# Kernel tuning notes

Hardware: AMD Instinct MI355X
Metric: run time of the kernel (lower is better)

The kernel has to match this reference:

```python
import jax, jax.numpy as jnp
import numpy as np

EPS = 1e-12  # torch F.normalize eps


def setup_inputs() -> dict:
    key = jax.random.key(0)
    k1, k2, k3, k4, k5 = jax.random.split(key, 5)
    N, C, H, W = 32, 512, 32, 32
    E = 1024   # expansion * dim
    G = 8      # group
    D = E // G # 128, per-group channel dim
    K = 64     # num_clusters
    x = jax.random.normal(k1, (N, C, H, W), dtype=jnp.float32)
    W1 = jax.random.normal(k2, (E, C), dtype=jnp.float32) / np.sqrt(C)
    W2 = jax.random.normal(k3, (G, E), dtype=jnp.float32) / np.sqrt(E)
    Wc = jax.random.normal(k4, (K, D), dtype=jnp.float32) / np.sqrt(D)
    centroids = jax.random.uniform(k5, (K, D), dtype=jnp.float32)
    return {"x": x, "W1": W1, "W2": W2, "Wc": Wc, "centroids": centroids}


def reference(x, W1, W2, Wc, centroids):
    # x: [N, C, H, W]; W1: [E, C]; W2: [G, E]; Wc: [K, D]; centroids: [K, D]
    N, C, H, W = x.shape
    E = W1.shape[0]
    G = W2.shape[0]
    K, D = Wc.shape
    P = H * W
    # descriptor-wise L2 normalization over channel dim
    norm = jnp.linalg.norm(x, axis=1, keepdims=True)
    x = x / jnp.maximum(norm, EPS)
    # linear1 on channels: [N, E, P]
    xe = jnp.einsum('ncp,ec->nep', x.reshape(N, C, P), W1)
    # grouped features: [N, G, D, P]
    xg = xe.reshape(N, G, D, P)
    # attention gate: sigmoid(linear2)  -> [N, G, P]
    att = jax.nn.sigmoid(jnp.einsum('nep,ge->ngp', xe, W2))
    # 1x1 conv = per-pixel matmul with cluster weights -> [N, G, K, P]
    soft_assign = jax.nn.softmax(jnp.einsum('ngdp,kd->ngkp', xg, Wc), axis=2)
    # combined per-(cluster,pixel) weight
    w = soft_assign * att[:, :, None, :]  # [N, G, K, P]
    # NetVLAD residual aggregation, algebraically decomposed to avoid the
    # giant [N,G,K,D,P] intermediate:
    #   vlad[n,k,d] = sum_{g,p} w * xg  -  centroids[k,d] * sum_{g,p} w
    agg = jnp.einsum('ngkp,ngdp->nkd', w, xg)  # [N, K, D]
    wsum = w.sum(axis=(1, 3))                  # [N, K]
    vlad = agg - wsum[:, :, None] * centroids[None]  # [N, K, D]
    return vlad.reshape(N, K * D)
```

## Files before the change

kernel.cpp:

```cpp
#include <hip/hip_runtime.h>


#define N_  32
#define C_  512
#define P_  1024
#define E_  1024
#define G_  8
#define D_  128
#define K_  64

typedef __attribute__((ext_vector_type(8))) short bf16x8;
typedef __attribute__((ext_vector_type(4))) float f32x4;

__device__ __forceinline__ unsigned short f2b(float f) {
    union { float f; unsigned u; } v; v.f = f;
    unsigned r = (v.u + 0x7FFFu + ((v.u >> 16) & 1u)) >> 16;
    return (unsigned short)r;
}
__device__ __forceinline__ float b2f(unsigned short h) {
    union { unsigned u; float f; } v; v.u = ((unsigned)h) << 16;
    return v.f;
}

__device__ __forceinline__ void gl_lds16(const void* g, void* l) {
    __builtin_amdgcn_global_load_lds(
        (const __attribute__((address_space(1))) void*)g,
        (__attribute__((address_space(3))) void*)l, 16, 0, 0);
}

#define SB  __builtin_amdgcn_sched_barrier(0)
#define BAR __builtin_amdgcn_s_barrier()

__global__ __launch_bounds__(256) void k0_prep(const float* __restrict__ W1,
                                               const float* __restrict__ Wc,
                                               unsigned short* __restrict__ W1b,
                                               unsigned short* __restrict__ Vb) {
    int bid = blockIdx.x;
    int t = threadIdx.x;
    int i0 = bid * 512 + t;
    W1b[i0]       = f2b(W1[i0]);
    W1b[i0 + 256] = f2b(W1[i0 + 256]);
    int ch = bid & 1, k = (bid >> 1) & 63, g = bid >> 7;
    int c = ch * 256 + t;
    float acc = 0.f;
    #pragma unroll 8
    for (int d = 0; d < 128; ++d)
        acc += Wc[k * 128 + d] * W1[(g * 128 + d) * C_ + c];
    Vb[(g * 64 + k) * C_ + c] = f2b(acc);
}

__global__ __launch_bounds__(256) void k1_norm_transpose(const float* __restrict__ x,
                                                         unsigned short* __restrict__ xhat_t) {
    __shared__ short xc[128 * 256];
    __shared__ float red[256];
    __shared__ float rn[64];
    int n = blockIdx.y;
    int p0 = blockIdx.x * 64;
    int t = threadIdx.x;
    int ps = t & 63, cs = t >> 6;

    float ss = 0.f;
    for (int i = 0; i < 128; ++i) {
        float v = x[((size_t)(n * C_ + cs * 128 + i)) * P_ + p0 + ps];
        ss += v * v;
        xc[i * 256 + t] = (short)f2b(v);
    }
    red[t] = ss;
    __syncthreads();
    if (t < 64) {
        float s = red[t] + red[64 + t] + red[128 + t] + red[192 + t];
        rn[t] = 1.0f / fmaxf(sqrtf(s), 1e-12f);
    }
    __syncthreads();

    float r = rn[ps];
    size_t base = ((size_t)(n * P_ + p0 + ps)) * C_ + cs * 128;
    #pragma unroll
    for (int jj = 0; jj < 16; ++jj) {
        bf16x8 o;
        #pragma unroll
        for (int j = 0; j < 8; ++j)
            o[j] = (short)f2b(b2f((unsigned short)xc[(jj * 8 + j) * 256 + t]) * r);
        *(bf16x8*)&xhat_t[base + jj * 8] = o;
    }
}

__global__ __launch_bounds__(256) void k2_gemm_xe(const unsigned short* __restrict__ W1b,
                                                  const unsigned short* __restrict__ xhat_t,
                                                  unsigned short* __restrict__ xe) {
    __shared__ __align__(16) short As[128 * 64];
    __shared__ __align__(16) short Bs[128 * 64];
    int n = blockIdx.y;
    int e0 = (blockIdx.x >> 3) * 128;
    int p0 = (blockIdx.x & 7) * 128;
    int t = threadIdx.x;
    int w = t >> 6, l = t & 63, q = l >> 4, l15 = l & 15;
    int wr = w >> 1, wc = w & 1;

    f32x4 acc[4][4];
    #pragma unroll
    for (int mi = 0; mi < 4; ++mi)
        #pragma unroll
        for (int ni = 0; ni < 4; ++ni)
            acc[mi][ni] = (f32x4){0.f, 0.f, 0.f, 0.f};

    for (int ks = 0; ks < 8; ++ks) {
        int k0 = ks * 64;
        #pragma unroll
        for (int i = 0; i < 4; ++i) {
            int ch = i * 256 + t;
            int row = ch >> 3, c8 = ch & 7;
            gl_lds16(&W1b[(e0 + row) * C_ + k0 + ((c8 ^ (row & 7)) * 8)], &As[ch * 8]);
        }
        #pragma unroll
        for (int i = 0; i < 4; ++i) {
            int ch = i * 256 + t;
            int row = ch >> 3, c8 = ch & 7;
            gl_lds16(&xhat_t[((size_t)(n * P_ + p0 + row)) * C_ + k0 + ((c8 ^ (row & 7)) * 8)], &Bs[ch * 8]);
        }
        __syncthreads();

        #pragma unroll
        for (int kk = 0; kk < 2; ++kk) {
            bf16x8 af[4], bf[4];
            #pragma unroll
            for (int mi = 0; mi < 4; ++mi)
                af[mi] = *(const bf16x8*)&As[(wr * 64 + mi * 16 + l15) * 64 + (((kk * 4 + q) ^ (l15 & 7)) * 8)];
            #pragma unroll
            for (int ni = 0; ni < 4; ++ni)
                bf[ni] = *(const bf16x8*)&Bs[(wc * 64 + ni * 16 + l15) * 64 + (((kk * 4 + q) ^ (l15 & 7)) * 8)];
            #pragma unroll
            for (int mi = 0; mi < 4; ++mi)
                #pragma unroll
                for (int ni = 0; ni < 4; ++ni)
                    acc[mi][ni] = __builtin_amdgcn_mfma_f32_16x16x32_bf16(af[mi], bf[ni], acc[mi][ni], 0, 0, 0);
        }
        __syncthreads();
    }

    #pragma unroll
    for (int mi = 0; mi < 4; ++mi) {
        #pragma unroll
        for (int ni = 0; ni < 4; ++ni) {
            #pragma unroll
            for (int r = 0; r < 4; ++r) {
                int e = e0 + wr * 64 + mi * 16 + q * 4 + r;
                int p = p0 + wc * 64 + ni * 16 + l15;
                xe[((size_t)(n * E_ + e)) * P_ + p] = f2b(acc[mi][ni][r]);
            }
        }
    }
}

__global__ __launch_bounds__(256) void k3a_att_part(const unsigned short* __restrict__ xe,
                                                    const float* __restrict__ W2,
                                                    float* __restrict__ att_part) {
    int n = blockIdx.y;
    int ec = blockIdx.x;
    int t = threadIdx.x;
    int e0 = ec * 64;
    f32x4 acc[8];
    #pragma unroll
    for (int g = 0; g < 8; ++g) acc[g] = (f32x4){0.f, 0.f, 0.f, 0.f};
    #pragma unroll 4
    for (int i = 0; i < 64; ++i) {
        int e = e0 + i;
        ushort4 v4 = *(const ushort4*)&xe[((size_t)(n * E_ + e)) * P_ + t * 4];
        f32x4 vf = {b2f(v4.x), b2f(v4.y), b2f(v4.z), b2f(v4.w)};
        #pragma unroll
        for (int g = 0; g < 8; ++g)
            acc[g] += vf * W2[g * E_ + e];
    }
    #pragma unroll
    for (int g = 0; g < 8; ++g)
        *(f32x4*)&att_part[(((size_t)(n * 16 + ec)) * 8 + g) * P_ + t * 4] = acc[g];
}

__global__ __launch_bounds__(256) void k3b_att_reduce(const float* __restrict__ att_part,
                                                      float* __restrict__ att_s) {
    int idx = blockIdx.x * 256 + threadIdx.x;
    int p = idx & 1023;
    int g = (idx >> 10) & 7;
    int n = idx >> 13;
    float s = 0.f;
    #pragma unroll
    for (int ec = 0; ec < 16; ++ec)
        s += att_part[(((size_t)(n * 16 + ec)) * 8 + g) * P_ + p];
    att_s[idx] = 1.0f / (1.0f + __expf(-s));
}

__device__ __forceinline__ void stage_s(short* sb, const unsigned short* __restrict__ Vb,
                                        const unsigned short* __restrict__ xhat_t,
                                        int g, int n, int p0c, int k0, int t) {
    {
        int row = t >> 3, c8 = t & 7;
        gl_lds16(&Vb[(g * 64 + row) * C_ + k0 + ((c8 ^ (row & 7)) * 8)], &sb[t * 8]);
    }
    #pragma unroll
    for (int i = 0; i < 2; ++i) {
        int ch = i * 512 + t;
        int row = ch >> 3, c8 = ch & 7;
        gl_lds16(&xhat_t[((size_t)(n * P_ + p0c + row)) * C_ + k0 + ((c8 ^ (row & 7)) * 8)],
                 &sb[4096 + ch * 8]);
    }
}

__device__ __forceinline__ void stage_xg(short* xglds, const unsigned short* __restrict__ xe,
                                         int n, int g, int p0c, int t) {
    #pragma unroll
    for (int i = 0; i < 4; ++i) {
        int ch = i * 512 + t;
        int row = ch >> 4, c16 = ch & 15;
        gl_lds16(&xe[((size_t)(n * E_ + g * 128 + row)) * P_ + p0c + ((c16 ^ (row & 7)) * 8)],
                 &xglds[ch * 8]);
    }
}

__device__ __forceinline__ void mfma_s(f32x4 acc[4], const short* sb, int w, int q, int l15) {
    #pragma unroll
    for (int kk = 0; kk < 2; ++kk) {
        bf16x8 af[4], bfr;
        #pragma unroll
        for (int mi = 0; mi < 4; ++mi)
            af[mi] = *(const bf16x8*)&sb[(mi * 16 + l15) * 64 + (((kk * 4 + q) ^ (l15 & 7)) * 8)];
        bfr = *(const bf16x8*)&sb[4096 + (w * 16 + l15) * 64 + (((kk * 4 + q) ^ (l15 & 7)) * 8)];
        #pragma unroll
        for (int mi = 0; mi < 4; ++mi)
            acc[mi] = __builtin_amdgcn_mfma_f32_16x16x32_bf16(af[mi], bfr, acc[mi], 0, 0, 0);
    }
}

__global__ __launch_bounds__(512, 4) void k4_assign_agg(const unsigned short* __restrict__ Vb,
                                                        const unsigned short* __restrict__ xhat_t,
                                                        const unsigned short* __restrict__ xe,
                                                        const float* __restrict__ att_s,
                                                        float* __restrict__ agg_part,
                                                        float* __restrict__ wsum_part) {
    __shared__ __align__(16) char smem[81920];
    short* S0    = (short*)smem;
    short* S1    = (short*)(smem + 24576);
    short* xglds = (short*)(smem + 49152);
    short* wlds  = (short*)smem;
    float* wred  = (float*)smem;

    int b = blockIdx.y * 16 + blockIdx.x;
    int work = (b & 7) * 64 + (b >> 3);
    int n = work >> 4, g = work & 7, ph = (work >> 3) & 1;

    int t = threadIdx.x;
    int w = t >> 6, l = t & 63, q = l >> 4, l15 = l & 15;
    int kh = w >> 2, dq = w & 3;

    f32x4 acc_a[2][2];
    #pragma unroll
    for (int mi = 0; mi < 2; ++mi)
        #pragma unroll
        for (int ni = 0; ni < 2; ++ni)
            acc_a[mi][ni] = (f32x4){0.f, 0.f, 0.f, 0.f};
    float wsp[16];
    #pragma unroll
    for (int j = 0; j < 16; ++j) wsp[j] = 0.f;

#define WAITV(n_) asm volatile("s_waitcnt vmcnt(" #n_ ")" ::: "memory")
#define RND(CUR, NXT, KN) \
    stage_s(NXT, Vb, xhat_t, g, n, p0c, (KN) * 64, t); \
    WAITV(3); BAR; SB; \
    mfma_s(acc_s, CUR, w, q, l15); \
    BAR; SB;

    #pragma unroll 1
    for (int cc = 0; cc < 4; ++cc) {
        int p0c = ph * 512 + cc * 128;

        float av = att_s[(((size_t)(n * G_ + g)) * P_) + p0c + w * 16 + l15];

        f32x4 acc_s[4];
        #pragma unroll
        for (int mi = 0; mi < 4; ++mi)
            acc_s[mi] = (f32x4){0.f, 0.f, 0.f, 0.f};

        stage_s(S0, Vb, xhat_t, g, n, p0c, 0, t);
        RND(S0, S1, 1)
        RND(S1, S0, 2)
        RND(S0, S1, 3)
        RND(S1, S0, 4)
        RND(S0, S1, 5)
        RND(S1, S0, 6)
        stage_s(S1, Vb, xhat_t, g, n, p0c, 448, t);
        stage_xg(xglds, xe, n, g, p0c, t);
        WAITV(7); BAR; SB;
        mfma_s(acc_s, S0, w, q, l15);
        BAR; SB;
        WAITV(4); BAR; SB;
        mfma_s(acc_s, S1, w, q, l15);
        BAR; SB;

        {
            float m = -1e30f;
            #pragma unroll
            for (int mi = 0; mi < 4; ++mi)
                #pragma unroll
                for (int r = 0; r < 4; ++r)
                    m = fmaxf(m, acc_s[mi][r]);
            m = fmaxf(m, __shfl_xor(m, 16));
            m = fmaxf(m, __shfl_xor(m, 32));
            float s = 0.f;
            #pragma unroll
            for (int mi = 0; mi < 4; ++mi)
                #pragma unroll
                for (int r = 0; r < 4; ++r) {
                    float e = __expf(acc_s[mi][r] - m);
                    acc_s[mi][r] = e;
                    s += e;
                }
            s += __shfl_xor(s, 16);
            s += __shfl_xor(s, 32);

            float scale = av / s;

            #pragma unroll
            for (int mi = 0; mi < 4; ++mi)
                #pragma unroll
                for (int r = 0; r < 4; ++r) {
                    float wv = acc_s[mi][r] * scale;
                    wsp[mi * 4 + r] += wv;
                    wlds[(mi * 16 + q * 4 + r) * 136 + (w * 16 + l15)] = (short)f2b(wv);
                }
        }
        __syncthreads();

        #pragma unroll
        for (int pk = 0; pk < 4; ++pk) {
            bf16x8 a2[2], b2[2];
            #pragma unroll
            for (int mi = 0; mi < 2; ++mi)
                a2[mi] = *(const bf16x8*)&wlds[(kh * 32 + mi * 16 + l15) * 136 + pk * 32 + q * 8];
            #pragma unroll
            for (int ni = 0; ni < 2; ++ni)
                b2[ni] = *(const bf16x8*)&xglds[(dq * 32 + ni * 16 + l15) * 128
                                                + (((pk * 4 + q) ^ (l15 & 7)) * 8)];
            #pragma unroll
            for (int mi = 0; mi < 2; ++mi)
                #pragma unroll
                for (int ni = 0; ni < 2; ++ni)
                    acc_a[mi][ni] = __builtin_amdgcn_mfma_f32_16x16x32_bf16(a2[mi], b2[ni], acc_a[mi][ni], 0, 0, 0);
        }
        __syncthreads();
    }

    size_t base = (((size_t)(n * G_ + g)) * 2 + ph) * 64;
    #pragma unroll
    for (int mi = 0; mi < 2; ++mi)
        #pragma unroll
        for (int ni = 0; ni < 2; ++ni)
            #pragma unroll
            for (int r = 0; r < 4; ++r) {
                int k = kh * 32 + mi * 16 + q * 4 + r;
                int d = dq * 32 + ni * 16 + l15;
                agg_part[(base + k) * 128 + d] = acc_a[mi][ni][r];
            }

    #pragma unroll
    for (int j = 0; j < 16; ++j) {
        float v = wsp[j];
        v += __shfl_xor(v, 1);
        v += __shfl_xor(v, 2);
        v += __shfl_xor(v, 4);
        v += __shfl_xor(v, 8);
        if (l15 == 0) {
            int k = (j >> 2) * 16 + q * 4 + (j & 3);
            wred[w * 64 + k] = v;
        }
    }
    __syncthreads();
    if (t < 64) {
        float s = 0.f;
        #pragma unroll
        for (int wv = 0; wv < 8; ++wv)
            s += wred[wv * 64 + t];
        wsum_part[(((size_t)(n * G_ + g)) * 2 + ph) * 64 + t] = s;
    }
}

__global__ __launch_bounds__(256) void k5_final(const float* __restrict__ agg_part,
                                                const float* __restrict__ wsum_part,
                                                const float* __restrict__ centroids,
                                                float* __restrict__ out) {
    int idx = blockIdx.x * 256 + threadIdx.x;
    int d = idx & 127;
    int k = (idx >> 7) & 63;
    int n = idx >> 13;
    float ws = 0.f;
    #pragma unroll
    for (int g = 0; g < 8; ++g)
        #pragma unroll
        for (int ph = 0; ph < 2; ++ph)
            ws += wsum_part[(((size_t)(n * G_ + g)) * 2 + ph) * 64 + k];
    float agg = 0.f;
    #pragma unroll
    for (int g = 0; g < 8; ++g)
        #pragma unroll
        for (int ph = 0; ph < 2; ++ph)
            agg += agg_part[(((((size_t)(n * G_ + g)) * 2 + ph) * 64) + k) * 128 + d];
    out[idx] = agg - ws * centroids[k * 128 + d];
}

extern "C" void kernel_launch(void* const* d_in, const int* in_sizes, int n_in,
                              void* d_out, int out_size, void* d_ws, size_t ws_size,
                              hipStream_t stream) {
    const float* x         = (const float*)d_in[0];
    const float* W1        = (const float*)d_in[1];
    const float* W2        = (const float*)d_in[2];
    const float* Wc        = (const float*)d_in[3];
    const float* centroids = (const float*)d_in[4];
    float* out = (float*)d_out;

    char* ws = (char*)d_ws;
    unsigned short* W1b      = (unsigned short*)(ws + 0);
    unsigned short* Vb       = (unsigned short*)(ws + 1048576);
    unsigned short* xhat_t   = (unsigned short*)(ws + 1572864);
    unsigned short* xe       = (unsigned short*)(ws + 35127296);
    float*          att_s    = (float*)(ws + 102236160);
    float*          att_part = (float*)(ws + 103284736);
    float*          agg_part = (float*)(ws + 103284736);
    float*          wsum_part= (float*)(ws + 120061952);

    hipLaunchKernelGGL(k0_prep,        dim3(1024), dim3(256), 0, stream, W1, Wc, W1b, Vb);
    hipLaunchKernelGGL(k1_norm_transpose, dim3(16, 32), dim3(256), 0, stream, x, xhat_t);
    hipLaunchKernelGGL(k2_gemm_xe,     dim3(64, 32), dim3(256), 0, stream, W1b, xhat_t, xe);
    hipLaunchKernelGGL(k3a_att_part,   dim3(16, 32), dim3(256), 0, stream, xe, W2, att_part);
    hipLaunchKernelGGL(k3b_att_reduce, dim3(1024), dim3(256), 0, stream, att_part, att_s);
    hipLaunchKernelGGL(k4_assign_agg,  dim3(16, 32), dim3(512), 0, stream, Vb, xhat_t, xe,
                       att_s, agg_part, wsum_part);
    hipLaunchKernelGGL(k5_final,       dim3(1024), dim3(256), 0, stream,
                       agg_part, wsum_part, centroids, out);
}
```

Measured before the change: 230.7 us.

## Fold W2 into W1 to compute attention gate directly from normalized input

Precomputes Wa = W2·W1 (8x512) in the prep kernel and computes the attention logits with a small MFMA GEMM over the normalized bf16 input, instead of reading the full E=1024 xe tensor and reducing partial sums in two kernels. This removes a large read of xe plus the att_part write/read round trip and one launch. Risk is slightly different rounding, since the folded weight is bf16, and the MFMA wastes half its rows on zero padding.

Measured after the change: 244.5 us. +6.0%, slower.

```diff
diff --git a/kernel.cpp b/kernel.cpp
--- a/kernel.cpp
+++ b/kernel.cpp
@@ -33,20 +33,33 @@
 
 __global__ __launch_bounds__(256) void k0_prep(const float* __restrict__ W1,
                                                const float* __restrict__ Wc,
+                                               const float* __restrict__ W2,
                                                unsigned short* __restrict__ W1b,
-                                               unsigned short* __restrict__ Vb) {
+                                               unsigned short* __restrict__ Vb,
+                                               unsigned short* __restrict__ Wa) {
     int bid = blockIdx.x;
     int t = threadIdx.x;
-    int i0 = bid * 512 + t;
-    W1b[i0]       = f2b(W1[i0]);
-    W1b[i0 + 256] = f2b(W1[i0 + 256]);
-    int ch = bid & 1, k = (bid >> 1) & 63, g = bid >> 7;
-    int c = ch * 256 + t;
-    float acc = 0.f;
-    #pragma unroll 8
-    for (int d = 0; d < 128; ++d)
-        acc += Wc[k * 128 + d] * W1[(g * 128 + d) * C_ + c];
-    Vb[(g * 64 + k) * C_ + c] = f2b(acc);
+    if (bid < 1024) {
+        int i0 = bid * 512 + t;
+        W1b[i0]       = f2b(W1[i0]);
+        W1b[i0 + 256] = f2b(W1[i0 + 256]);
+        int ch = bid & 1, k = (bid >> 1) & 63, g = bid >> 7;
+        int c = ch * 256 + t;
+        float acc = 0.f;
+        #pragma unroll 8
+        for (int d = 0; d < 128; ++d)
+            acc += Wc[k * 128 + d] * W1[(g * 128 + d) * C_ + c];
+        Vb[(g * 64 + k) * C_ + c] = f2b(acc);
+    } else {
+        int b2 = bid - 1024;
+        int g = b2 >> 1, ch = b2 & 1;
+        int c = ch * 256 + t;
+        float acc = 0.f;
+        #pragma unroll 8
+        for (int e = 0; e < 1024; ++e)
+            acc += W2[g * E_ + e] * W1[e * C_ + c];
+        Wa[g * C_ + c] = f2b(acc);
+    }
 }
 
 __global__ __launch_bounds__(256) void k1_norm_transpose(const float* __restrict__ x,
@@ -152,41 +165,50 @@
     }
 }
 
-__global__ __launch_bounds__(256) void k3a_att_part(const unsigned short* __restrict__ xe,
-                                                    const float* __restrict__ W2,
-                                                    float* __restrict__ att_part) {
+__global__ __launch_bounds__(256) void k3n_att(const unsigned short* __restrict__ Wa,
+                                               const unsigned short* __restrict__ xhat_t,
+                                               float* __restrict__ att_s) {
+    __shared__ __align__(16) short xh[64 * 512];
+    __shared__ __align__(16) short wal[8 * 520];
     int n = blockIdx.y;
-    int ec = blockIdx.x;
+    int p0 = blockIdx.x * 64;
     int t = threadIdx.x;
-    int e0 = ec * 64;
-    f32x4 acc[8];
-    #pragma unroll
-    for (int g = 0; g < 8; ++g) acc[g] = (f32x4){0.f, 0.f, 0.f, 0.f};
-    #pragma unroll 4
-    for (int i = 0; i < 64; ++i) {
-        int e = e0 + i;
-        ushort4 v4 = *(const ushort4*)&xe[((size_t)(n * E_ + e)) * P_ + t * 4];
-        f32x4 vf = {b2f(v4.x), b2f(v4.y), b2f(v4.z), b2f(v4.w)};
-        #pragma unroll
-        for (int g = 0; g < 8; ++g)
-            acc[g] += vf * W2[g * E_ + e];
-    }
-    #pragma unroll
-    for (int g = 0; g < 8; ++g)
-        *(f32x4*)&att_part[(((size_t)(n * 16 + ec)) * 8 + g) * P_ + t * 4] = acc[g];
-}
-
-__global__ __launch_bounds__(256) void k3b_att_reduce(const float* __restrict__ att_part,
-                                                      float* __restrict__ att_s) {
-    int idx = blockIdx.x * 256 + threadIdx.x;
-    int p = idx & 1023;
-    int g = (idx >> 10) & 7;
-    int n = idx >> 13;
-    float s = 0.f;
-    #pragma unroll
-    for (int ec = 0; ec < 16; ++ec)
-        s += att_part[(((size_t)(n * 16 + ec)) * 8 + g) * P_ + p];
-    att_s[idx] = 1.0f / (1.0f + __expf(-s));
+    int w = t >> 6, l = t & 63, q = l >> 4, l15 = l & 15;
+
+    #pragma unroll
+    for (int i = 0; i < 16; ++i) {
+        int ch = i * 256 + t;
+        int row = ch >> 6, s = ch & 63;
+        gl_lds16(&xhat_t[((size_t)(n * P_ + p0 + row)) * C_ + ((s ^ (row & 7)) * 8)],
+                 &xh[ch * 8]);
+    }
+    #pragma unroll
+    for (int i = 0; i < 2; ++i) {
+        int ch = i * 256 + t;
+        int row = ch >> 6, c8 = ch & 63;
+        gl_lds16(&Wa[row * C_ + c8 * 8], &wal[row * 520 + c8 * 8]);
+    }
+    __syncthreads();
+
+    f32x4 acc = (f32x4){0.f, 0.f, 0.f, 0.f};
+    const bf16x8 zf = {};
+    #pragma unroll
+    for (int kstep = 0; kstep < 16; ++kstep) {
+        bf16x8 av = *(const bf16x8*)&wal[(l15 & 7) * 520 + (kstep * 4 + q) * 8];
+        bf16x8 af = (l15 < 8) ? av : zf;
+        int row = w * 16 + l15;
+        bf16x8 bf = *(const bf16x8*)&xh[row * 512 + (((kstep * 4 + q) ^ (row & 7)) * 8)];
+        acc = __builtin_amdgcn_mfma_f32_16x16x32_bf16(af, bf, acc, 0, 0, 0);
+    }
+
+    if (q < 2) {
+        int p = p0 + w * 16 + l15;
+        #pragma unroll
+        for (int r = 0; r < 4; ++r) {
+            int g = q * 4 + r;
+            att_s[((size_t)(n * G_ + g)) * P_ + p] = 1.0f / (1.0f + __expf(-acc[r]));
+        }
+    }
 }
 
 __device__ __forceinline__ void stage_s(short* sb, const unsigned short* __restrict__ Vb,
@@ -421,15 +443,14 @@
     unsigned short* xhat_t   = (unsigned short*)(ws + 1572864);
     unsigned short* xe       = (unsigned short*)(ws + 35127296);
     float*          att_s    = (float*)(ws + 102236160);
-    float*          att_part = (float*)(ws + 103284736);
     float*          agg_part = (float*)(ws + 103284736);
     float*          wsum_part= (float*)(ws + 120061952);
-
-    hipLaunchKernelGGL(k0_prep,        dim3(1024), dim3(256), 0, stream, W1, Wc, W1b, Vb);
+    unsigned short* Wa       = (unsigned short*)(ws + 120193024);
+
+    hipLaunchKernelGGL(k0_prep,        dim3(1040), dim3(256), 0, stream, W1, Wc, W2, W1b, Vb, Wa);
     hipLaunchKernelGGL(k1_norm_transpose, dim3(16, 32), dim3(256), 0, stream, x, xhat_t);
     hipLaunchKernelGGL(k2_gemm_xe,     dim3(64, 32), dim3(256), 0, stream, W1b, xhat_t, xe);
-    hipLaunchKernelGGL(k3a_att_part,   dim3(16, 32), dim3(256), 0, stream, xe, W2, att_part);
-    hipLaunchKernelGGL(k3b_att_reduce, dim3(1024), dim3(256), 0, stream, att_part, att_s);
+    hipLaunchKernelGGL(k3n_att,        dim3(16, 32), dim3(256), 0, stream, Wa, xhat_t, att_s);
     hipLaunchKernelGGL(k4_assign_agg,  dim3(16, 32), dim3(512), 0, stream, Vb, xhat_t, xe,
                        att_s, agg_part, wsum_part);
     hipLaunchKernelGGL(k5_final,       dim3(1024), dim3(256), 0, stream,
```
